# Kernel optimization log

Measured on AMD Instinct MI355X. Metric: run time of the kernel, lower is better.

The kernel has to match this reference:

```python
import jax, jax.numpy as jnp
import numpy as np

N, E, G = 8000, 128000, 4
C, NLM, NL = 64, 16, 4
NEL, NB, NH = 10, 8, 64
RMAX = 5.0
PCUT = 5.0
AVG_NEIGH = 16.0
SIGMA = 1.0
LBOX = 6.0
KR = 3
T = 2
LMAP = jnp.array([0, 1, 1, 1, 2, 2, 2, 2, 2, 3, 3, 3, 3, 3, 3, 3])


def _nvec():
    r = np.arange(-KR, KR + 1)
    n = np.stack(np.meshgrid(r, r, r, indexing='ij'), -1).reshape(-1, 3)
    n = n[np.any(n != 0, axis=1)]  # [342,3], k=0 excluded
    return jnp.asarray(n, jnp.float32)


def sph_harm(u):
    # component-normalized real spherical harmonics up to l=3, unit input u [E,3]
    x, y, z = u[:, 0], u[:, 1], u[:, 2]
    one = jnp.ones_like(x)
    c3, c5, c15 = 3.0 ** 0.5, 5.0 ** 0.5, 15.0 ** 0.5
    Y = [one,
         c3 * x, c3 * y, c3 * z,
         c15 * x * y, c15 * y * z, 0.5 * c5 * (3 * z * z - 1.0), c15 * x * z, 0.5 * c15 * (x * x - y * y),
         (35.0 / 8.0) ** 0.5 * y * (3 * x * x - y * y), 105.0 ** 0.5 * x * y * z,
         (21.0 / 8.0) ** 0.5 * y * (5 * z * z - 1.0), 0.5 * 7.0 ** 0.5 * z * (5 * z * z - 3.0),
         (21.0 / 8.0) ** 0.5 * x * (5 * z * z - 1.0), 0.5 * 105.0 ** 0.5 * z * (x * x - y * y),
         (35.0 / 8.0) ** 0.5 * x * (x * x - 3 * y * y)]
    return jnp.stack(Y, -1)  # [E,16]


def radial_basis(r):
    # Bessel basis * polynomial cutoff (MACE RadialEmbeddingBlock)
    u = r / RMAX
    n = jnp.arange(1, NB + 1, dtype=jnp.float32)
    bes = (2.0 / RMAX) ** 0.5 * jnp.sin(n[None, :] * jnp.pi * u[:, None]) / (r[:, None] + 1e-9)
    p = PCUT
    fc = 1.0 - 0.5 * (p + 1) * (p + 2) * u ** p + p * (p + 2) * u ** (p + 1) - 0.5 * p * (p + 1) * u ** (p + 2)
    fc = fc * (u < 1.0)
    return bes * fc[:, None]  # [E,8]


def setup_inputs() -> dict:
    key = jax.random.key(0)
    ks = jax.random.split(key, 24)

    def p(k, shape, fan_in):
        return jax.random.normal(k, shape, jnp.float32) / (fan_in ** 0.5)

    elem = jax.random.randint(ks[0], (N,), 0, NEL)
    inp = {
        'node_attrs': jax.nn.one_hot(elem, NEL, dtype=jnp.float32),
        'positions': jax.random.uniform(ks[1], (N, 3), jnp.float32) * LBOX,
        'shifts': jnp.zeros((E, 3), jnp.float32),
        'density_coefficients': jax.random.normal(ks[2], (N, 1), jnp.float32) * 0.1,
        'cell': jnp.tile(jnp.eye(3, dtype=jnp.float32) * LBOX, (G, 1, 1)),
        'rcell': jnp.tile(jnp.eye(3, dtype=jnp.float32) / LBOX, (G, 1, 1)),
        'volume': jnp.full((G,), LBOX ** 3, jnp.float32),
        'edge_index': jax.random.randint(ks[3], (2, E), 0, N),
        'batch': jnp.repeat(jnp.arange(G), N // G),
        'emb_W': p(ks[4], (NEL, C), NEL),
        'q_coef': p(ks[5], (T, C), 1),
        'rad_W1': p(ks[6], (T, NB, NH), NB),
        'rad_W2': p(ks[7], (T, NH, NH), NH),
        'rad_W3': p(ks[8], (T, NH, NH), NH),
        'rad_W4': p(ks[9], (T, NH, C * NL), NH),
        'lin_up': p(ks[10], (T, NL, C, C), C),
        'lin_out': p(ks[11], (T, NL, C, C), C),
        'W_sc': p(ks[12], (T, NEL, C, C), C),
        'Wp': p(ks[13], (T, 3, C, C), C),
        'W_read0': p(ks[14], (C,), C),
        'Wread1_a': p(ks[15], (C, 16), C),
        'Wread1_b': p(ks[16], (16,), 16),
        'Wq_read': p(ks[17], (T, C), C),
        'atomic_E': jax.random.normal(ks[18], (NEL,), jnp.float32),
    }
    return inp


def reference(node_attrs, positions, shifts, density_coefficients, cell, rcell, volume,
              edge_index, batch, emb_W, q_coef, rad_W1, rad_W2, rad_W3, rad_W4,
              lin_up, lin_out, W_sc, Wp, W_read0, Wread1_a, Wread1_b, Wq_read, atomic_E):
    sender, receiver = edge_index[0], edge_index[1]
    vec = positions[receiver] - positions[sender] + shifts
    r = jnp.linalg.norm(vec, axis=-1)
    Y = sph_harm(vec / (r[:, None] + 1e-9))      # [E,16]
    ef = radial_basis(r)                          # [E,8]

    q = density_coefficients                      # [N,1], max_l=0 multipoles
    feats = jnp.zeros((N, C, NLM), jnp.float32).at[:, :, 0].set(node_attrs @ emb_W)
    e0 = jax.ops.segment_sum(node_attrs @ atomic_E, batch, G)
    energies = [e0]

    for t in range(T):
        # charge-coefficient injection (charge_coefs_linears)
        feats = feats.at[:, :, 0].add(q * q_coef[t][None, :])
        # per-l linear up
        h = jnp.einsum('ncl,lcd->ndl', feats, lin_up[t][LMAP])
        # radial MLP -> per-edge, per-channel, per-l tensor-product weights
        w = jax.nn.silu(ef @ rad_W1[t])
        w = jax.nn.silu(w @ rad_W2[t])
        w = jax.nn.silu(w @ rad_W3[t])
        w = (w @ rad_W4[t]).reshape(E, C, NL)[:, :, LMAP]   # [E,C,16]
        # depthwise equivariant TP message: gather -> contract -> modulate
        hj = h[sender]                                       # [E,C,16]
        s_e = jnp.einsum('ecl,el->ec', hj, Y)                # edge invariant
        m = w * (Y[:, None, :] * s_e[:, :, None])            # [E,C,16]
        A = jax.ops.segment_sum(m, receiver, N) / AVG_NEIGH  # scatter-reduce
        A = jnp.einsum('ncl,lcd->ndl', A, lin_out[t][LMAP])
        # element-dependent residual (self-connection)
        wn = jnp.einsum('nk,kcd->ncd', node_attrs, W_sc[t])
        sc = jnp.einsum('ncd,ncl->ndl', wn, feats)
        # product block: correlation-3 symmetric-contraction surrogate
        s1 = jnp.sum(A * A, axis=2)                           # [N,C]
        out = (jnp.einsum('ncl,cd->ndl', A, Wp[t, 0])
               + jnp.einsum('ncl,cd->ndl', A * s1[:, :, None], Wp[t, 1])
               + jnp.einsum('ncl,cd->ndl', A * (s1 * s1)[:, :, None], Wp[t, 2]))
        feats = out + sc
        # readout
        if t == T - 1:
            node_e = jax.nn.silu(feats[:, :, 0] @ Wread1_a) @ Wread1_b
        else:
            node_e = feats[:, :, 0] @ W_read0
        node_e = node_e + q[:, 0] * (feats[:, :, 0] @ Wq_read[t])
        energies.append(jax.ops.segment_sum(node_e, batch, G))

    # k-space (Ewald-like) electrostatics with Gaussian-smeared charges
    nv = _nvec()                                              # [K,3]
    kvec = 2.0 * jnp.pi * jnp.einsum('kj,gji->gki', nv, rcell)  # [G,K,3]
    k2 = jnp.sum(kvec * kvec, -1)                             # [G,K]
    phase = jnp.einsum('ni,nki->nk', positions, kvec[batch])  # [N,K]
    Sr = jax.ops.segment_sum(q * jnp.cos(phase), batch, G)
    Si = jax.ops.segment_sum(q * jnp.sin(phase), batch, G)
    filt = jnp.exp(-0.5 * SIGMA * SIGMA * k2) / k2
    Ees = (2.0 * jnp.pi / volume) * jnp.sum(filt * (Sr * Sr + Si * Si), axis=1)

    total_energy = jnp.sum(jnp.stack(energies, -1), -1) + Ees
    total_charge = jax.ops.segment_sum(q[:, 0], batch, G)
    dipole = jax.ops.segment_sum(q * positions, batch, G)
    return total_energy, total_charge, dipole
```

## Files before the change

### kernel.cpp

```cpp
#include <hip/hip_runtime.h>
#include <hip/hip_bf16.h>

constexpr int N    = 8000;
constexpr int E    = 128000;
constexpr int G    = 4;
constexpr int NEL  = 10;
constexpr int NGR  = N / G;
constexpr int NC   = N * 64;
constexpr int NK   = 342;
constexpr float RMAX = 5.0f;
constexpr int HS = 72;
constexpr int WT_T = 25088;

typedef __bf16 bf16x8 __attribute__((ext_vector_type(8)));
typedef float  f32x4v __attribute__((ext_vector_type(4)));
typedef unsigned short u16x8 __attribute__((ext_vector_type(8)));

__device__ __forceinline__ int lmap_rt(int l) { return (l >= 1) + (l >= 4) + (l >= 9); }
__device__ __forceinline__ float silu(float x) { return x / (1.f + __expf(-x)); }
__device__ __forceinline__ float bf2f(unsigned short u) { return __uint_as_float(((unsigned)u) << 16); }
__device__ __forceinline__ unsigned short f2bf(float f) {
    __hip_bfloat16 h = __float2bfloat16(f);
    return *(unsigned short*)&h;
}

__device__ __forceinline__ void mfma_stage(const unsigned short* hsrc, const unsigned short* wt,
                                           int m0, int lane, f32x4v acc[4], bool k8only)
{
    const int quad = lane >> 4;
    const int idx  = lane & 15;
    bf16x8 bz;
    #pragma unroll
    for (int i = 0; i < 8; ++i) bz[i] = (__bf16)0.f;
    bf16x8 a0 = bz, a1 = bz;
    const int mrow = m0 + idx;
    if (k8only) {
        if (quad == 0) a0 = *(const bf16x8*)&hsrc[mrow * HS];
    } else {
        a0 = *(const bf16x8*)&hsrc[mrow * HS + (quad << 3)];
        a1 = *(const bf16x8*)&hsrc[mrow * HS + 32 + (quad << 3)];
    }
    #pragma unroll
    for (int c4 = 0; c4 < 4; ++c4) {
        const int nrow = (c4 << 4) + idx;
        if (k8only) {
            bf16x8 b0 = bz;
            if (quad == 0) b0 = *(const bf16x8*)&wt[nrow * HS];
            acc[c4] = __builtin_amdgcn_mfma_f32_16x16x32_bf16(a0, b0, acc[c4], 0, 0, 0);
        } else {
            const bf16x8 b0 = *(const bf16x8*)&wt[nrow * HS + (quad << 3)];
            const bf16x8 b1 = *(const bf16x8*)&wt[nrow * HS + 32 + (quad << 3)];
            acc[c4] = __builtin_amdgcn_mfma_f32_16x16x32_bf16(a0, b0, acc[c4], 0, 0, 0);
            acc[c4] = __builtin_amdgcn_mfma_f32_16x16x32_bf16(a1, b1, acc[c4], 0, 0, 0);
        }
    }
}

__global__ __launch_bounds__(256) void k_init(const float* __restrict__ na,
    const float* __restrict__ q, const float* __restrict__ pos,
    const int* __restrict__ batch, const float* __restrict__ aE,
    int* __restrict__ elem, int* __restrict__ counts, float* __restrict__ acc)
{
    __shared__ float s[G * 5];
    if (threadIdx.x < G * 5) s[threadIdx.x] = 0.f;
    __syncthreads();
    const int n = blockIdx.x * 256 + threadIdx.x;
    if (n < N) {
        int el = 0; float best = na[n * NEL];
        #pragma unroll
        for (int j = 1; j < NEL; ++j) { float v = na[n * NEL + j]; if (v > best) { best = v; el = j; } }
        elem[n] = el;
        atomicAdd(&counts[el], 1);
        const int g = batch[n];
        const float qn = q[n];
        atomicAdd(&s[g * 5 + 0], aE[el]);
        atomicAdd(&s[g * 5 + 1], qn);
        atomicAdd(&s[g * 5 + 2], qn * pos[n * 3 + 0]);
        atomicAdd(&s[g * 5 + 3], qn * pos[n * 3 + 1]);
        atomicAdd(&s[g * 5 + 4], qn * pos[n * 3 + 2]);
    }
    __syncthreads();
    if (threadIdx.x < G * 5) atomicAdd(&acc[threadIdx.x], s[threadIdx.x]);
}

__global__ __launch_bounds__(256) void k_feat0(const int* __restrict__ elem,
    const float* __restrict__ embW, float* __restrict__ F)
{
    const int i = blockIdx.x * 256 + threadIdx.x;
    if (i < NC) F[i] = embW[elem[i >> 6] * 64 + (i & 63)];
}

__global__ void k_offs(const int* __restrict__ counts, int* __restrict__ offs)
{
    if (threadIdx.x == 0 && blockIdx.x == 0) {
        int o = 0;
        for (int j = 0; j < NEL; ++j) { offs[j] = o; o += (counts[j] + 63) & ~63; }
        offs[NEL] = o;
    }
}
__global__ __launch_bounds__(256) void k_scatter(const int* __restrict__ elem,
    const int* __restrict__ offs, int* __restrict__ cursor, int* __restrict__ perm)
{
    const int n = blockIdx.x * 256 + threadIdx.x;
    if (n < N) {
        const int el = elem[n];
        const int p = atomicAdd(&cursor[el], 1);
        perm[offs[el] + p] = n;
    }
}

__global__ __launch_bounds__(256) void k_gcnt(const int* __restrict__ ei, int* __restrict__ cnt)
{
    const int e = blockIdx.x * 256 + threadIdx.x;
    if (e < E) atomicAdd(&cnt[ei[E + e]], 1);
}
__global__ __launch_bounds__(1024) void k_goff(const int* __restrict__ cnt, int* __restrict__ roff)
{
    __shared__ int part[1024];
    const int t = threadIdx.x;
    const int base = t * 8;
    int loc[8];
    int s = 0;
    #pragma unroll
    for (int i = 0; i < 8; ++i) { loc[i] = s; s += (base + i < N) ? cnt[base + i] : 0; }
    part[t] = s;
    __syncthreads();
    for (int d = 1; d < 1024; d <<= 1) {
        const int v = (t >= d) ? part[t - d] : 0;
        __syncthreads();
        part[t] += v;
        __syncthreads();
    }
    const int excl = (t == 0) ? 0 : part[t - 1];
    #pragma unroll
    for (int i = 0; i < 8; ++i) if (base + i < N) roff[base + i] = excl + loc[i];
    if (t == 0) roff[N] = E;
}
__global__ __launch_bounds__(256) void k_gscat(const int* __restrict__ ei,
    const int* __restrict__ roff, int* __restrict__ cur, int* __restrict__ elist)
{
    const int e = blockIdx.x * 256 + threadIdx.x;
    if (e < E) {
        const int rv = ei[E + e];
        const int p = atomicAdd(&cur[rv], 1);
        elist[roff[rv] + p] = e;
    }
}

__global__ __launch_bounds__(256) void k_geom(const float* __restrict__ pos,
    const float* __restrict__ shifts, const int* __restrict__ ei,
    const int* __restrict__ elist, float4* __restrict__ geomv, int* __restrict__ spck)
{
    const int j = blockIdx.x * 256 + threadIdx.x;
    if (j >= E) return;
    const int e = elist[j];
    const int s = ei[e], rv = ei[E + e];
    const float dx = pos[rv * 3 + 0] - pos[s * 3 + 0] + shifts[e * 3 + 0];
    const float dy = pos[rv * 3 + 1] - pos[s * 3 + 1] + shifts[e * 3 + 1];
    const float dz = pos[rv * 3 + 2] - pos[s * 3 + 2] + shifts[e * 3 + 2];
    const float r = sqrtf(dx * dx + dy * dy + dz * dz);
    const float inv = 1.f / (r + 1e-9f);
    float4 g;
    g.x = dx * inv; g.y = dy * inv; g.z = dz * inv; g.w = r;
    geomv[j] = g;
    spck[j] = s;
}

__global__ __launch_bounds__(256) void k_wprep_all(const float* __restrict__ rW1,
    const float* __restrict__ rW2, const float* __restrict__ rW3,
    const float* __restrict__ rW4, const float* __restrict__ Wp,
    const float* __restrict__ lup, const float* __restrict__ lout,
    const float* __restrict__ Wsc,
    unsigned short* __restrict__ WT, unsigned short* __restrict__ WpT,
    unsigned short* __restrict__ WlupT, unsigned short* __restrict__ WloutT,
    unsigned short* __restrict__ WscT)
{
    const int gidx = blockIdx.x * 256 + threadIdx.x;
    if (gidx < 2 * WT_T) {
        const int t = gidx / WT_T;
        const int r = gidx % WT_T;
        float v;
        if (r < 512) {
            const int n = r >> 3, k = r & 7;
            v = rW1[t * 512 + k * 64 + n];
        } else if (r < 4608) {
            const int i = r - 512, n = i >> 6, k = i & 63;
            v = rW2[t * 4096 + k * 64 + n];
        } else if (r < 8704) {
            const int i = r - 4608, n = i >> 6, k = i & 63;
            v = rW3[t * 4096 + k * 64 + n];
        } else {
            const int i = r - 8704, n = i >> 6, k = i & 63;
            v = rW4[t * 16384 + k * 256 + n];
        }
        WT[gidx] = f2bf(v);
    } else if (gidx < 2 * WT_T + 24576) {
        const int idx = gidx - 2 * WT_T;
        const int i  = idx & 4095;
        const int d = i >> 6, c = i & 63;
        WpT[idx] = f2bf(Wp[(size_t)(idx >> 12) * 4096 + c * 64 + d]);
    } else if (gidx < 2 * WT_T + 24576 + 32768) {
        const int idx = gidx - (2 * WT_T + 24576);
        const int i = idx & 4095, d = i >> 6, c = i & 63;
        WlupT[idx] = f2bf(lup[(idx >> 12) * 4096 + c * 64 + d]);
    } else if (gidx < 2 * WT_T + 24576 + 65536) {
        const int idx = gidx - (2 * WT_T + 24576 + 32768);
        const int i = idx & 4095, d = i >> 6, c = i & 63;
        WloutT[idx] = f2bf(lout[(idx >> 12) * 4096 + c * 64 + d]);
    } else if (gidx < 2 * WT_T + 24576 + 65536 + 81920) {
        const int idx = gidx - (2 * WT_T + 24576 + 65536);
        const int i = idx & 4095, d = i >> 6, c = i & 63;
        WscT[idx] = f2bf(Wsc[(idx >> 12) * 4096 + c * 64 + d]);
    }
}

__global__ __launch_bounds__(256) void k_lgemm_hb(float* __restrict__ F,
    const float* __restrict__ q, const float* __restrict__ qc,
    const unsigned short* __restrict__ WT, unsigned short* __restrict__ Hb)
{
    __shared__ unsigned short Xb[64 * HS];
    __shared__ unsigned short Wt[64 * HS];
    const int l  = blockIdx.y;
    const int nb = blockIdx.x << 6;
    const int t  = threadIdx.x;
    const int lane = t & 63;
    const int m0   = (t >> 6) << 4;
    const int quad = lane >> 4;
    const int idx  = lane & 15;
    const int prow = t >> 2, pkb = (t & 3) << 4;
    float* Xp = F + (size_t)l * NC + (size_t)nb * 64;
    if (l == 0) {
        #pragma unroll
        for (int k = 0; k < 16; ++k) {
            const int i = t + (k << 8);
            float v = Xp[i] + q[nb + (i >> 6)] * qc[i & 63];
            Xp[i] = v;
            Xb[(i >> 6) * HS + (i & 63)] = f2bf(v);
        }
    } else {
        #pragma unroll
        for (int k = 0; k < 16; ++k) {
            const int i = t + (k << 8);
            Xb[(i >> 6) * HS + (i & 63)] = f2bf(Xp[i]);
        }
    }
    const unsigned short* W = WT + lmap_rt(l) * 4096;
    *(u16x8*)&Wt[prow * HS + pkb]     = *(const u16x8*)&W[prow * 64 + pkb];
    *(u16x8*)&Wt[prow * HS + pkb + 8] = *(const u16x8*)&W[prow * 64 + pkb + 8];
    __syncthreads();
    f32x4v acc[4];
    #pragma unroll
    for (int c = 0; c < 4; ++c) { acc[c][0] = 0.f; acc[c][1] = 0.f; acc[c][2] = 0.f; acc[c][3] = 0.f; }
    mfma_stage(Xb, Wt, m0, lane, acc, false);
    #pragma unroll
    for (int c4 = 0; c4 < 4; ++c4) {
        #pragma unroll
        for (int r = 0; r < 4; ++r) {
            const int n = nb + m0 + (quad << 2) + r;
            const int col = (c4 << 4) + idx;
            Hb[(size_t)n * 1024 + (l << 6) + col] = f2bf(acc[c4][r]);
        }
    }
}

__global__ __launch_bounds__(256) void k_hbT(const unsigned short* __restrict__ Hb,
    unsigned short* __restrict__ HbT)
{
    const int n = (blockIdx.x << 2) + (threadIdx.x >> 6);
    const int c = threadIdx.x & 63;
    u16x8 a, b;
    #pragma unroll
    for (int l = 0; l < 8; ++l) {
        a[l] = Hb[(size_t)n * 1024 + (l << 6) + c];
        b[l] = Hb[(size_t)n * 1024 + ((l + 8) << 6) + c];
    }
    *(u16x8*)&HbT[(size_t)n * 1024 + c * 16]     = a;
    *(u16x8*)&HbT[(size_t)n * 1024 + c * 16 + 8] = b;
}

__global__ __launch_bounds__(256) void k_lgemm(const float* __restrict__ X,
    const unsigned short* __restrict__ WT, float* __restrict__ Out)
{
    __shared__ unsigned short Xb[64 * HS];
    __shared__ unsigned short Wt[64 * HS];
    const int l  = blockIdx.y;
    const int nb = blockIdx.x << 6;
    const int t  = threadIdx.x;
    const int lane = t & 63;
    const int m0   = (t >> 6) << 4;
    const int quad = lane >> 4;
    const int idx  = lane & 15;
    const int prow = t >> 2, pkb = (t & 3) << 4;
    const float* Xp = X + (size_t)l * NC + (size_t)nb * 64;
    #pragma unroll
    for (int k = 0; k < 16; ++k) {
        const int i = t + (k << 8);
        Xb[(i >> 6) * HS + (i & 63)] = f2bf(Xp[i]);
    }
    const unsigned short* W = WT + lmap_rt(l) * 4096;
    *(u16x8*)&Wt[prow * HS + pkb]     = *(const u16x8*)&W[prow * 64 + pkb];
    *(u16x8*)&Wt[prow * HS + pkb + 8] = *(const u16x8*)&W[prow * 64 + pkb + 8];
    __syncthreads();
    f32x4v acc[4];
    #pragma unroll
    for (int c = 0; c < 4; ++c) { acc[c][0] = 0.f; acc[c][1] = 0.f; acc[c][2] = 0.f; acc[c][3] = 0.f; }
    mfma_stage(Xb, Wt, m0, lane, acc, false);
    float* Op = Out + (size_t)l * NC + (size_t)nb * 64;
    #pragma unroll
    for (int c4 = 0; c4 < 4; ++c4) {
        #pragma unroll
        for (int r = 0; r < 4; ++r) {
            const int row = m0 + (quad << 2) + r;
            Op[(row << 6) + (c4 << 4) + idx] = acc[c4][r];
        }
    }
}

__global__ __launch_bounds__(256) void k_sc(const float* __restrict__ F,
    const unsigned short* __restrict__ WscT, const int* __restrict__ perm,
    const int* __restrict__ elem, float* __restrict__ Out)
{
    __shared__ unsigned short Xb[64 * HS];
    __shared__ unsigned short Wt[64 * HS];
    __shared__ int rows[64];
    const int l  = blockIdx.y;
    const int tb = blockIdx.x << 6;
    const int t  = threadIdx.x;
    if (t < 64) rows[t] = perm[tb + t];
    __syncthreads();
    if (rows[0] < 0) return;
    const int lane = t & 63;
    const int m0   = (t >> 6) << 4;
    const int quad = lane >> 4;
    const int idx  = lane & 15;
    const int prow = t >> 2, pkb = (t & 3) << 4;
    const unsigned short* W = WscT + elem[rows[0]] * 4096;
    *(u16x8*)&Wt[prow * HS + pkb]     = *(const u16x8*)&W[prow * 64 + pkb];
    *(u16x8*)&Wt[prow * HS + pkb + 8] = *(const u16x8*)&W[prow * 64 + pkb + 8];
    #pragma unroll
    for (int k = 0; k < 16; ++k) {
        const int i = t + (k << 8);
        const int rr = i >> 6, cc = i & 63;
        const int n = rows[rr];
        Xb[rr * HS + cc] = (n >= 0) ? f2bf(F[(size_t)l * NC + (size_t)n * 64 + cc]) : (unsigned short)0;
    }
    __syncthreads();
    f32x4v acc[4];
    #pragma unroll
    for (int c = 0; c < 4; ++c) { acc[c][0] = 0.f; acc[c][1] = 0.f; acc[c][2] = 0.f; acc[c][3] = 0.f; }
    mfma_stage(Xb, Wt, m0, lane, acc, false);
    #pragma unroll
    for (int c4 = 0; c4 < 4; ++c4) {
        #pragma unroll
        for (int r = 0; r < 4; ++r) {
            const int n = rows[m0 + (quad << 2) + r];
            if (n >= 0) Out[(size_t)l * NC + (size_t)n * 64 + (c4 << 4) + idx] = acc[c4][r];
        }
    }
}

__global__ __launch_bounds__(256) void k_wgemm(const float4* __restrict__ geomv,
    const unsigned short* __restrict__ WT, unsigned short* __restrict__ wout)
{
    __shared__ unsigned short hbf[64 * HS];
    __shared__ unsigned short wtb[2][64 * HS];
    __shared__ unsigned short outS[64 * HS];
    const int t = threadIdx.x;
    const int lane = t & 63;
    const int wid  = t >> 6;
    const int m0   = wid << 4;
    const int quad = lane >> 4;
    const int idx  = lane & 15;
    const int j0 = blockIdx.x << 6;
    if (t < 64) {
        const float r = geomv[j0 + t].w;
        const float u  = r * 0.2f;
        const float u2 = u * u, u5 = u2 * u2 * u;
        const float fc = 1.f - 21.f * u5 + 35.f * u5 * u - 15.f * u5 * u2;
        float pref = 0.63245553f * fc / (r + 1e-9f);
        if (u >= 1.f) pref = 0.f;
        const float piu = 3.14159265358979f * u;
        #pragma unroll
        for (int b = 0; b < 8; ++b) hbf[t * HS + b] = f2bf(__sinf((float)(b + 1) * piu) * pref);
    }
    {
        const int n = t >> 2, k = (t & 3) << 1;
        wtb[0][n * HS + k]     = WT[n * 8 + k];
        wtb[0][n * HS + k + 1] = WT[n * 8 + k + 1];
    }
    const int prow = t >> 2, pkb = (t & 3) << 4;
    u16x8 pf0, pf1;
    pf0 = *(const u16x8*)&WT[512 + prow * 64 + pkb];
    pf1 = *(const u16x8*)&WT[512 + prow * 64 + pkb + 8];
    __syncthreads();
    f32x4v acc[4];
    #pragma unroll
    for (int c = 0; c < 4; ++c) { acc[c][0] = 0.f; acc[c][1] = 0.f; acc[c][2] = 0.f; acc[c][3] = 0.f; }
    mfma_stage(hbf, wtb[0], m0, lane, acc, true);
    __syncthreads();
    #pragma unroll
    for (int c4 = 0; c4 < 4; ++c4)
        #pragma unroll
        for (int r = 0; r < 4; ++r)
            hbf[(m0 + (quad << 2) + r) * HS + (c4 << 4) + idx] = f2bf(silu(acc[c4][r]));
    *(u16x8*)&wtb[1][prow * HS + pkb]     = pf0;
    *(u16x8*)&wtb[1][prow * HS + pkb + 8] = pf1;
    pf0 = *(const u16x8*)&WT[4608 + prow * 64 + pkb];
    pf1 = *(const u16x8*)&WT[4608 + prow * 64 + pkb + 8];
    __syncthreads();
    #pragma unroll
    for (int c = 0; c < 4; ++c) { acc[c][0] = 0.f; acc[c][1] = 0.f; acc[c][2] = 0.f; acc[c][3] = 0.f; }
    mfma_stage(hbf, wtb[1], m0, lane, acc, false);
    __syncthreads();
    #pragma unroll
    for (int c4 = 0; c4 < 4; ++c4)
        #pragma unroll
        for (int r = 0; r < 4; ++r)
            hbf[(m0 + (quad << 2) + r) * HS + (c4 << 4) + idx] = f2bf(silu(acc[c4][r]));
    *(u16x8*)&wtb[0][prow * HS + pkb]     = pf0;
    *(u16x8*)&wtb[0][prow * HS + pkb + 8] = pf1;
    pf0 = *(const u16x8*)&WT[8704 + prow * 64 + pkb];
    pf1 = *(const u16x8*)&WT[8704 + prow * 64 + pkb + 8];
    __syncthreads();
    #pragma unroll
    for (int c = 0; c < 4; ++c) { acc[c][0] = 0.f; acc[c][1] = 0.f; acc[c][2] = 0.f; acc[c][3] = 0.f; }
    mfma_stage(hbf, wtb[0], m0, lane, acc, false);
    __syncthreads();
    #pragma unroll
    for (int c4 = 0; c4 < 4; ++c4)
        #pragma unroll
        for (int r = 0; r < 4; ++r)
            hbf[(m0 + (quad << 2) + r) * HS + (c4 << 4) + idx] = f2bf(silu(acc[c4][r]));
    *(u16x8*)&wtb[1][prow * HS + pkb]     = pf0;
    *(u16x8*)&wtb[1][prow * HS + pkb + 8] = pf1;
    pf0 = *(const u16x8*)&WT[8704 + 4096 + prow * 64 + pkb];
    pf1 = *(const u16x8*)&WT[8704 + 4096 + prow * 64 + pkb + 8];
    __syncthreads();
    int cur = 1;
    for (int c = 0; c < 4; ++c) {
        #pragma unroll
        for (int cc = 0; cc < 4; ++cc) { acc[cc][0] = 0.f; acc[cc][1] = 0.f; acc[cc][2] = 0.f; acc[cc][3] = 0.f; }
        mfma_stage(hbf, wtb[cur], m0, lane, acc, false);
        __syncthreads();
        #pragma unroll
        for (int c4 = 0; c4 < 4; ++c4)
            #pragma unroll
            for (int r = 0; r < 4; ++r)
                outS[(m0 + (quad << 2) + r) * HS + (c4 << 4) + idx] = f2bf(acc[c4][r]);
        if (c < 3) {
            *(u16x8*)&wtb[1 - cur][prow * HS + pkb]     = pf0;
            *(u16x8*)&wtb[1 - cur][prow * HS + pkb + 8] = pf1;
            if (c < 2) {
                pf0 = *(const u16x8*)&WT[8704 + (c + 2) * 4096 + prow * 64 + pkb];
                pf1 = *(const u16x8*)&WT[8704 + (c + 2) * 4096 + prow * 64 + pkb + 8];
            }
        }
        __syncthreads();
        *(u16x8*)&wout[(size_t)(j0 + prow) * 256 + (c << 6) + pkb]     = *(const u16x8*)&outS[prow * HS + pkb];
        *(u16x8*)&wout[(size_t)(j0 + prow) * 256 + (c << 6) + pkb + 8] = *(const u16x8*)&outS[prow * HS + pkb + 8];
        cur ^= 1;
    }
}

__global__ __launch_bounds__(256) void k_agg(const float4* __restrict__ geomv,
    const int* __restrict__ spck,
    const unsigned short* __restrict__ HbT, const unsigned short* __restrict__ wb,
    const int* __restrict__ roff, float* __restrict__ A)
{
    const int lane = threadIdx.x & 63;
    const int n = (blockIdx.x << 2) + (threadIdx.x >> 6);
    const int ja = roff[n], jb2 = roff[n + 1];
    float accv[16];
    #pragma unroll
    for (int l = 0; l < 16; ++l) accv[l] = 0.f;
    constexpr int LM[16] = {0,1,1,1,2,2,2,2,2,3,3,3,3,3,3,3};
    if (ja < jb2) {
        const int jlast = jb2 - 1;
        int j1c = ja + 1 < jlast ? ja + 1 : jlast;
        int j2c = ja + 2 < jlast ? ja + 2 : jlast;
        float4 g0 = geomv[ja],  g1 = geomv[j1c],  g2 = geomv[j2c];
        ushort4 w0 = *(const ushort4*)&wb[(size_t)ja * 256 + (lane << 2)];
        ushort4 w1 = *(const ushort4*)&wb[(size_t)j1c * 256 + (lane << 2)];
        ushort4 w2 = *(const ushort4*)&wb[(size_t)j2c * 256 + (lane << 2)];
        int sB = spck[j1c], sC = spck[j2c];
        u16x8 hA, hB;
        {
            const int s0 = spck[ja];
            hA = *(const u16x8*)&HbT[(size_t)s0 * 1024 + lane * 16];
            hB = *(const u16x8*)&HbT[(size_t)s0 * 1024 + lane * 16 + 8];
        }
        for (int j = ja; j < jb2; ++j) {
            const float4 gc = g0;
            const ushort4 wc = w0;
            float hc[16];
            #pragma unroll
            for (int l = 0; l < 8; ++l) { hc[l] = bf2f(hA[l]); hc[l + 8] = bf2f(hB[l]); }
            g0 = g1; g1 = g2; w0 = w1; w1 = w2;
            const int sA = sB; sB = sC;
            hA = *(const u16x8*)&HbT[(size_t)sA * 1024 + lane * 16];
            hB = *(const u16x8*)&HbT[(size_t)sA * 1024 + lane * 16 + 8];
            const int j3 = j + 3 < jlast ? j + 3 : jlast;
            g2 = geomv[j3];
            w2 = *(const ushort4*)&wb[(size_t)j3 * 256 + (lane << 2)];
            sC = spck[j3];
            if (gc.w < RMAX) {
                const float x = gc.x, y = gc.y, z = gc.z;
                const float xx = x * x, yy = y * y, zz = z * z;
                float Y[16];
                Y[0] = 1.f;
                Y[1] = 1.7320508f * x;  Y[2] = 1.7320508f * y;  Y[3] = 1.7320508f * z;
                Y[4] = 3.8729833f * x * y;  Y[5] = 3.8729833f * y * z;
                Y[6] = 0.5f * 2.2360680f * (3.f * zz - 1.f);
                Y[7] = 3.8729833f * x * z;  Y[8] = 0.5f * 3.8729833f * (xx - yy);
                Y[9]  = 2.0916500f * y * (3.f * xx - yy);
                Y[10] = 10.2469508f * x * y * z;
                Y[11] = 1.6201852f * y * (5.f * zz - 1.f);
                Y[12] = 0.5f * 2.6457513f * z * (5.f * zz - 3.f);
                Y[13] = 1.6201852f * x * (5.f * zz - 1.f);
                Y[14] = 0.5f * 10.2469508f * z * (xx - yy);
                Y[15] = 2.0916500f * x * (xx - 3.f * yy);
                float se = 0.f;
                #pragma unroll
                for (int l = 0; l < 16; ++l) se += hc[l] * Y[l];
                se *= 0.0625f;
                const float wl[4] = { bf2f(wc.x) * se, bf2f(wc.y) * se, bf2f(wc.z) * se, bf2f(wc.w) * se };
                #pragma unroll
                for (int l = 0; l < 16; ++l) accv[l] += wl[LM[l]] * Y[l];
            }
        }
    }
    float* Ap = A + (size_t)n * 64 + lane;
    #pragma unroll
    for (int l = 0; l < 16; ++l) Ap[(size_t)l * NC] = accv[l];
}

__global__ __launch_bounds__(256) void k_s1(const float* __restrict__ H, float* __restrict__ s1)
{
    const int i = blockIdx.x * 256 + threadIdx.x;
    if (i < NC) {
        float s = 0.f;
        #pragma unroll
        for (int l = 0; l < 16; ++l) { const float a = H[(size_t)l * NC + i]; s += a * a; }
        s1[i] = s;
    }
}

__global__ __launch_bounds__(256) void k_out(const float* __restrict__ Ap,
    const float* __restrict__ s1, const unsigned short* __restrict__ WpT,
    const float* __restrict__ sc, float* __restrict__ F)
{
    __shared__ unsigned short Xb[64 * HS];
    __shared__ unsigned short Wt[64 * HS];
    const int l  = blockIdx.y;
    const int nb = blockIdx.x << 6;
    const int t  = threadIdx.x;
    const int lane = t & 63;
    const int m0   = (t >> 6) << 4;
    const int quad = lane >> 4;
    const int idx  = lane & 15;
    const int prow = t >> 2, pkb = (t & 3) << 4;
    const float* Xp = Ap + (size_t)l * NC + (size_t)nb * 64;
    float av[16], sv[16];
    #pragma unroll
    for (int k = 0; k < 16; ++k) {
        const int i = t + (k << 8);
        av[k] = Xp[i];
        sv[k] = s1[nb * 64 + i];
    }
    f32x4v acc[4];
    #pragma unroll
    for (int c = 0; c < 4; ++c) { acc[c][0] = 0.f; acc[c][1] = 0.f; acc[c][2] = 0.f; acc[c][3] = 0.f; }
    for (int p = 0; p < 3; ++p) {
        #pragma unroll
        for (int k = 0; k < 16; ++k) {
            const int i = t + (k << 8);
            Xb[(i >> 6) * HS + (i & 63)] = f2bf(av[k]);
            av[k] *= sv[k];
        }
        *(u16x8*)&Wt[prow * HS + pkb]     = *(const u16x8*)&WpT[p * 4096 + prow * 64 + pkb];
        *(u16x8*)&Wt[prow * HS + pkb + 8] = *(const u16x8*)&WpT[p * 4096 + prow * 64 + pkb + 8];
        __syncthreads();
        mfma_stage(Xb, Wt, m0, lane, acc, false);
        __syncthreads();
    }
    #pragma unroll
    for (int c4 = 0; c4 < 4; ++c4) {
        #pragma unroll
        for (int r = 0; r < 4; ++r) {
            const int row = m0 + (quad << 2) + r;
            const int col = (c4 << 4) + idx;
            const size_t id = (size_t)l * NC + (size_t)(nb + row) * 64 + col;
            F[id] = acc[c4][r] + sc[id];
        }
    }
}

__global__ __launch_bounds__(256) void k_read(const float* __restrict__ F,
    const float* __restrict__ q, const int* __restrict__ batch,
    const float* __restrict__ Wr0, const float* __restrict__ Wa,
    const float* __restrict__ Wb, const float* __restrict__ Wq,
    float* __restrict__ acc, int last)
{
    __shared__ float sred[G];
    if (threadIdx.x < G) sred[threadIdx.x] = 0.f;
    __syncthreads();
    const int n = blockIdx.x * 256 + threadIdx.x;
    if (n < N) {
        float a16[16];
        #pragma unroll
        for (int j = 0; j < 16; ++j) a16[j] = 0.f;
        float ar = 0.f, aq = 0.f;
        const float* f = F + (size_t)n * 64;
        for (int c = 0; c < 64; ++c) {
            const float fv = f[c];
            aq += fv * Wq[c];
            if (last) {
                #pragma unroll
                for (int j = 0; j < 16; ++j) a16[j] += fv * Wa[c * 16 + j];
            } else ar += fv * Wr0[c];
        }
        float en;
        if (last) {
            en = 0.f;
            #pragma unroll
            for (int j = 0; j < 16; ++j) en += silu(a16[j]) * Wb[j];
        } else en = ar;
        en += q[n] * aq;
        atomicAdd(&sred[batch[n]], en);
    }
    __syncthreads();
    if (threadIdx.x < G) atomicAdd(&acc[threadIdx.x * 5], sred[threadIdx.x]);
}

__global__ __launch_bounds__(256) void k_kvec(const float* __restrict__ rcell,
    float* __restrict__ kvec, float* __restrict__ k2)
{
    const int idx = blockIdx.x * 256 + threadIdx.x;
    if (idx >= G * NK) return;
    const int g = idx / NK, k = idx % NK;
    const int kk = k + (k >= 171 ? 1 : 0);
    const int a = kk / 49 - 3, b = (kk / 7) % 7 - 3, c = kk % 7 - 3;
    const float* rc = rcell + g * 9;
    float s = 0.f;
    #pragma unroll
    for (int i = 0; i < 3; ++i) {
        const float kv = 6.283185307f * ((float)a * rc[0 + i] + (float)b * rc[3 + i] + (float)c * rc[6 + i]);
        kvec[idx * 3 + i] = kv;
        s += kv * kv;
    }
    k2[idx] = s;
}

__global__ __launch_bounds__(256) void k_phase(const float* __restrict__ pos,
    const float* __restrict__ q, const float* __restrict__ kvec,
    float* __restrict__ Sr, float* __restrict__ Si)
{
    __shared__ float kvs[38 * 3];
    __shared__ float srs[38], sis[38];
    const int g = blockIdx.z, kc = blockIdx.x, ncb = blockIdx.y;
    const int kbase = kc * 38;
    if (threadIdx.x < 38 * 3) kvs[threadIdx.x] = kvec[((size_t)g * NK + kbase) * 3 + threadIdx.x];
    if (threadIdx.x < 38) { srs[threadIdx.x] = 0.f; sis[threadIdx.x] = 0.f; }
    __syncthreads();
    const int t = threadIdx.x;
    float px = 0.f, py = 0.f, pz = 0.f, qn = 0.f;
    if (t < 250) {
        const int n = g * NGR + ncb * 250 + t;
        px = pos[n * 3]; py = pos[n * 3 + 1]; pz = pos[n * 3 + 2]; qn = q[n];
    }
    const int lane = t & 63;
    for (int j = 0; j < 38; ++j) {
        const float ph = px * kvs[j * 3] + py * kvs[j * 3 + 1] + pz * kvs[j * 3 + 2];
        float sv, cv;
        __sincosf(ph, &sv, &cv);
        float vr = qn * cv, vi = qn * sv;
        #pragma unroll
        for (int o = 32; o > 0; o >>= 1) { vr += __shfl_down(vr, o, 64); vi += __shfl_down(vi, o, 64); }
        if (lane == 0) { atomicAdd(&srs[j], vr); atomicAdd(&sis[j], vi); }
    }
    __syncthreads();
    if (t < 38) {
        atomicAdd(&Sr[g * NK + kbase + t], srs[t]);
        atomicAdd(&Si[g * NK + kbase + t], sis[t]);
    }
}

__global__ __launch_bounds__(512) void k_final(const float* __restrict__ k2,
    const float* __restrict__ Sr, const float* __restrict__ Si,
    const float* __restrict__ vol, const float* __restrict__ acc,
    float* __restrict__ out)
{
    __shared__ float red[512];
    const int g = blockIdx.x, t = threadIdx.x;
    float v = 0.f;
    if (t < NK) {
        const float kk = k2[g * NK + t];
        const float sr = Sr[g * NK + t], si = Si[g * NK + t];
        v = __expf(-0.5f * kk) * (sr * sr + si * si) / kk;
    }
    red[t] = v;
    __syncthreads();
    for (int s2 = 256; s2 > 0; s2 >>= 1) {
        if (t < s2) red[t] += red[t + s2];
        __syncthreads();
    }
    if (t == 0) {
        const float Ees = 6.283185307f / vol[g] * red[0];
        out[g]     = acc[g * 5 + 0] + Ees;
        out[4 + g] = acc[g * 5 + 1];
        out[8 + g * 3 + 0] = acc[g * 5 + 2];
        out[8 + g * 3 + 1] = acc[g * 5 + 3];
        out[8 + g * 3 + 2] = acc[g * 5 + 4];
    }
}

extern "C" void kernel_launch(void* const* d_in, const int* in_sizes, int n_in,
                              void* d_out, int out_size, void* d_ws, size_t ws_size,
                              hipStream_t stream)
{
    const float* na    = (const float*)d_in[0];
    const float* pos   = (const float*)d_in[1];
    const float* shif  = (const float*)d_in[2];
    const float* q     = (const float*)d_in[3];
    const float* rcell = (const float*)d_in[5];
    const float* vol   = (const float*)d_in[6];
    const int*   ei    = (const int*)d_in[7];
    const int*   batch = (const int*)d_in[8];
    const float* embW  = (const float*)d_in[9];
    const float* qcoef = (const float*)d_in[10];
    const float* rW1   = (const float*)d_in[11];
    const float* rW2   = (const float*)d_in[12];
    const float* rW3   = (const float*)d_in[13];
    const float* rW4   = (const float*)d_in[14];
    const float* lup   = (const float*)d_in[15];
    const float* lout  = (const float*)d_in[16];
    const float* Wsc   = (const float*)d_in[17];
    const float* Wp    = (const float*)d_in[18];
    const float* Wr0   = (const float*)d_in[19];
    const float* Wa    = (const float*)d_in[20];
    const float* Wb    = (const float*)d_in[21];
    const float* Wq    = (const float*)d_in[22];
    const float* aE    = (const float*)d_in[23];
    float* out = (float*)d_out;

    float* wsf  = (float*)d_ws;
    float* F    = wsf;
    float* A    = F + 8192000;
    float* R    = A + 8192000;
    float* H2   = R;
    unsigned short* Hbtmp = (unsigned short*)A;
    unsigned short* HbT   = (unsigned short*)R;
    unsigned short* wb = (unsigned short*)(R + 4096000);
    float* s1   = R + 20480000;
    float* kvec = s1 + 512000;
    float* k2   = kvec + 4104;
    float* Sr   = k2 + 1368;
    float* Si   = Sr + 1368;
    float* acc  = Si + 1368;
    int*   elem = (int*)(acc + 32);
    int*   perm = elem + 8000;
    int*   counts = perm + 8640;
    int*   cursor = counts + 16;
    int*   offs   = cursor + 16;
    int*   roff   = offs + 16;
    int*   cnt    = roff + 8001;
    int*   cur    = cnt + 8000;
    int*   elist  = cur + 8000;
    unsigned short* WTb = (unsigned short*)(((uintptr_t)(elist + E) + 31) & ~(uintptr_t)31);
    unsigned short* WpT = WTb + 2 * WT_T;
    float4* geomv = (float4*)(WpT + 24576);
    int*    spck  = (int*)(geomv + E);
    unsigned short* WlupT  = (unsigned short*)(spck + E);
    unsigned short* WloutT = WlupT + 32768;
    unsigned short* WscT   = WloutT + 32768;

    hipMemsetAsync(F, 0, 8192000 * sizeof(float), stream);
    hipMemsetAsync(Sr, 0, (1368 * 2 + 32) * sizeof(float), stream);
    hipMemsetAsync(perm, 0xFF, 8640 * sizeof(int), stream);
    hipMemsetAsync(counts, 0, 32 * sizeof(int), stream);
    hipMemsetAsync(cnt, 0, 16000 * sizeof(int), stream);

    k_init<<<32, 256, 0, stream>>>(na, q, pos, batch, aE, elem, counts, acc);
    k_feat0<<<2000, 256, 0, stream>>>(elem, embW, F);
    k_offs<<<1, 64, 0, stream>>>(counts, offs);
    k_scatter<<<32, 256, 0, stream>>>(elem, offs, cursor, perm);
    k_gcnt<<<500, 256, 0, stream>>>(ei, cnt);
    k_goff<<<1, 1024, 0, stream>>>(cnt, roff);
    k_gscat<<<500, 256, 0, stream>>>(ei, roff, cur, elist);
    k_geom<<<500, 256, 0, stream>>>(pos, shif, ei, elist, geomv, spck);
    k_wprep_all<<<868, 256, 0, stream>>>(rW1, rW2, rW3, rW4, Wp, lup, lout, Wsc,
                                         WTb, WpT, WlupT, WloutT, WscT);
    k_kvec<<<6, 256, 0, stream>>>(rcell, kvec, k2);
    k_phase<<<dim3(9, 8, G), 256, 0, stream>>>(pos, q, kvec, Sr, Si);

    for (int t = 0; t < 2; ++t) {
        k_lgemm_hb<<<dim3(125, 16), 256, 0, stream>>>(F, q, qcoef + t * 64, WlupT + t * 16384, Hbtmp);
        k_hbT<<<2000, 256, 0, stream>>>(Hbtmp, HbT);
        k_wgemm<<<2000, 256, 0, stream>>>(geomv, WTb + t * WT_T, wb);
        k_agg<<<2000, 256, 0, stream>>>(geomv, spck, HbT, wb, roff, A);
        k_lgemm<<<dim3(125, 16), 256, 0, stream>>>(A, WloutT + t * 16384, H2);
        k_s1<<<2000, 256, 0, stream>>>(H2, s1);
        k_sc<<<dim3(135, 16), 256, 0, stream>>>(F, WscT + t * 40960, perm, elem, A);
        k_out<<<dim3(125, 16), 256, 0, stream>>>(H2, s1, WpT + t * 12288, A, F);
        k_read<<<32, 256, 0, stream>>>(F, q, batch, Wr0, Wa, Wb, Wq + t * 64, acc, t == 1);
    }
    k_final<<<G, 512, 0, stream>>>(k2, Sr, Si, vol, acc, out);
}
```

Baseline: 573.1 us.

## Fuse radial weight MLP with edge aggregation, keeping per-edge weights in LDS

```diff
diff --git a/kernel.cpp b/kernel.cpp
--- a/kernel.cpp
+++ b/kernel.cpp
@@ -10,6 +10,7 @@
 constexpr int NK   = 342;
 constexpr float RMAX = 5.0f;
 constexpr int HS = 72;
+constexpr int WS2 = 260;
 constexpr int WT_T = 25088;
 
 typedef __bf16 bf16x8 __attribute__((ext_vector_type(8)));
@@ -359,21 +360,41 @@
     }
 }
 
-__global__ __launch_bounds__(256) void k_wgemm(const float4* __restrict__ geomv,
-    const unsigned short* __restrict__ WT, unsigned short* __restrict__ wout)
+__global__ __launch_bounds__(256) void k_edge(const float4* __restrict__ geomv,
+    const int* __restrict__ spck, const unsigned short* __restrict__ WT,
+    const unsigned short* __restrict__ HbT, const int* __restrict__ roff,
+    float* __restrict__ A)
 {
     __shared__ unsigned short hbf[64 * HS];
-    __shared__ unsigned short wtb[2][64 * HS];
-    __shared__ unsigned short outS[64 * HS];
+    __shared__ unsigned short wtb[64 * HS];
+    __shared__ unsigned short wfull[64 * WS2];
+    __shared__ float geos[64 * 4];
+    __shared__ int   sps[64];
+    __shared__ int   rinfo[2];
     const int t = threadIdx.x;
     const int lane = t & 63;
     const int wid  = t >> 6;
     const int m0   = wid << 4;
     const int quad = lane >> 4;
     const int idx  = lane & 15;
-    const int j0 = blockIdx.x << 6;
+    const int prow = t >> 2, pkb = (t & 3) << 4;
+    const int w0 = blockIdx.x << 6;
+    const int w1 = w0 + 64;
+    if (t == 0) {
+        int lo = 0, hi = N - 1;
+        while (lo < hi) { const int mid = (lo + hi + 1) >> 1; if (roff[mid] <= w0) lo = mid; else hi = mid - 1; }
+        rinfo[0] = lo;
+    } else if (t == 1) {
+        const int w1m = w0 + 63;
+        int lo = 0, hi = N - 1;
+        while (lo < hi) { const int mid = (lo + hi + 1) >> 1; if (roff[mid] <= w1m) lo = mid; else hi = mid - 1; }
+        rinfo[1] = lo;
+    }
     if (t < 64) {
-        const float r = geomv[j0 + t].w;
+        const float4 g = geomv[w0 + t];
+        *(float4*)&geos[t * 4] = g;
+        sps[t] = spck[w0 + t];
+        const float r = g.w;
         const float u  = r * 0.2f;
         const float u2 = u * u, u5 = u2 * u2 * u;
         const float fc = 1.f - 21.f * u5 + 35.f * u5 * u - 15.f * u5 * u2;
@@ -385,126 +406,111 @@
     }
     {
         const int n = t >> 2, k = (t & 3) << 1;
-        wtb[0][n * HS + k]     = WT[n * 8 + k];
-        wtb[0][n * HS + k + 1] = WT[n * 8 + k + 1];
-    }
-    const int prow = t >> 2, pkb = (t & 3) << 4;
-    u16x8 pf0, pf1;
-    pf0 = *(const u16x8*)&WT[512 + prow * 64 + pkb];
-    pf1 = *(const u16x8*)&WT[512 + prow * 64 + pkb + 8];
+        wtb[n * HS + k]     = WT[n * 8 + k];
+        wtb[n * HS + k + 1] = WT[n * 8 + k + 1];
+    }
+    u16x8 pf0 = *(const u16x8*)&WT[512 + prow * 64 + pkb];
+    u16x8 pf1 = *(const u16x8*)&WT[512 + prow * 64 + pkb + 8];
     __syncthreads();
     f32x4v acc[4];
     #pragma unroll
     for (int c = 0; c < 4; ++c) { acc[c][0] = 0.f; acc[c][1] = 0.f; acc[c][2] = 0.f; acc[c][3] = 0.f; }
-    mfma_stage(hbf, wtb[0], m0, lane, acc, true);
+    mfma_stage(hbf, wtb, m0, lane, acc, true);
     __syncthreads();
     #pragma unroll
     for (int c4 = 0; c4 < 4; ++c4)
         #pragma unroll
         for (int r = 0; r < 4; ++r)
             hbf[(m0 + (quad << 2) + r) * HS + (c4 << 4) + idx] = f2bf(silu(acc[c4][r]));
-    *(u16x8*)&wtb[1][prow * HS + pkb]     = pf0;
-    *(u16x8*)&wtb[1][prow * HS + pkb + 8] = pf1;
+    *(u16x8*)&wtb[prow * HS + pkb]     = pf0;
+    *(u16x8*)&wtb[prow * HS + pkb + 8] = pf1;
     pf0 = *(const u16x8*)&WT[4608 + prow * 64 + pkb];
     pf1 = *(const u16x8*)&WT[4608 + prow * 64 + pkb + 8];
     __syncthreads();
     #pragma unroll
     for (int c = 0; c < 4; ++c) { acc[c][0] = 0.f; acc[c][1] = 0.f; acc[c][2] = 0.f; acc[c][3] = 0.f; }
-    mfma_stage(hbf, wtb[1], m0, lane, acc, false);
+    mfma_stage(hbf, wtb, m0, lane, acc, false);
     __syncthreads();
     #pragma unroll
     for (int c4 = 0; c4 < 4; ++c4)
         #pragma unroll
         for (int r = 0; r < 4; ++r)
             hbf[(m0 + (quad << 2) + r) * HS + (c4 << 4) + idx] = f2bf(silu(acc[c4][r]));
-    *(u16x8*)&wtb[0][prow * HS + pkb]     = pf0;
-    *(u16x8*)&wtb[0][prow * HS + pkb + 8] = pf1;
+    *(u16x8*)&wtb[prow * HS + pkb]     = pf0;
+    *(u16x8*)&wtb[prow * HS + pkb + 8] = pf1;
     pf0 = *(const u16x8*)&WT[8704 + prow * 64 + pkb];
     pf1 = *(const u16x8*)&WT[8704 + prow * 64 + pkb + 8];
     __syncthreads();
     #pragma unroll
     for (int c = 0; c < 4; ++c) { acc[c][0] = 0.f; acc[c][1] = 0.f; acc[c][2] = 0.f; acc[c][3] = 0.f; }
-    mfma_stage(hbf, wtb[0], m0, lane, acc, false);
+    mfma_stage(hbf, wtb, m0, lane, acc, false);
     __syncthreads();
     #pragma unroll
     for (int c4 = 0; c4 < 4; ++c4)
         #pragma unroll
         for (int r = 0; r < 4; ++r)
             hbf[(m0 + (quad << 2) + r) * HS + (c4 << 4) + idx] = f2bf(silu(acc[c4][r]));
-    *(u16x8*)&wtb[1][prow * HS + pkb]     = pf0;
-    *(u16x8*)&wtb[1][prow * HS + pkb + 8] = pf1;
+    *(u16x8*)&wtb[prow * HS + pkb]     = pf0;
+    *(u16x8*)&wtb[prow * HS + pkb + 8] = pf1;
     pf0 = *(const u16x8*)&WT[8704 + 4096 + prow * 64 + pkb];
     pf1 = *(const u16x8*)&WT[8704 + 4096 + prow * 64 + pkb + 8];
     __syncthreads();
-    int cur = 1;
-    for (int c = 0; c < 4; ++c) {
-        #pragma unroll
-        for (int cc = 0; cc < 4; ++cc) { acc[cc][0] = 0.f; acc[cc][1] = 0.f; acc[cc][2] = 0.f; acc[cc][3] = 0.f; }
-        mfma_stage(hbf, wtb[cur], m0, lane, acc, false);
+    for (int cc = 0; cc < 4; ++cc) {
+        #pragma unroll
+        for (int c = 0; c < 4; ++c) { acc[c][0] = 0.f; acc[c][1] = 0.f; acc[c][2] = 0.f; acc[c][3] = 0.f; }
+        mfma_stage(hbf, wtb, m0, lane, acc, false);
         __syncthreads();
         #pragma unroll
         for (int c4 = 0; c4 < 4; ++c4)
             #pragma unroll
             for (int r = 0; r < 4; ++r)
-                outS[(m0 + (quad << 2) + r) * HS + (c4 << 4) + idx] = f2bf(acc[c4][r]);
-        if (c < 3) {
-            *(u16x8*)&wtb[1 - cur][prow * HS + pkb]     = pf0;
-            *(u16x8*)&wtb[1 - cur][prow * HS + pkb + 8] = pf1;
-            if (c < 2) {
-                pf0 = *(const u16x8*)&WT[8704 + (c + 2) * 4096 + prow * 64 + pkb];
-                pf1 = *(const u16x8*)&WT[8704 + (c + 2) * 4096 + prow * 64 + pkb + 8];
+                wfull[(m0 + (quad << 2) + r) * WS2 + (cc << 6) + (c4 << 4) + idx] = f2bf(acc[c4][r]);
+        if (cc < 3) {
+            *(u16x8*)&wtb[prow * HS + pkb]     = pf0;
+            *(u16x8*)&wtb[prow * HS + pkb + 8] = pf1;
+            if (cc < 2) {
+                pf0 = *(const u16x8*)&WT[8704 + (cc + 2) * 4096 + prow * 64 + pkb];
+                pf1 = *(const u16x8*)&WT[8704 + (cc + 2) * 4096 + prow * 64 + pkb + 8];
             }
         }
         __syncthreads();
-        *(u16x8*)&wout[(size_t)(j0 + prow) * 256 + (c << 6) + pkb]     = *(const u16x8*)&outS[prow * HS + pkb];
-        *(u16x8*)&wout[(size_t)(j0 + prow) * 256 + (c << 6) + pkb + 8] = *(const u16x8*)&outS[prow * HS + pkb + 8];
-        cur ^= 1;
-    }
-}
-
-__global__ __launch_bounds__(256) void k_agg(const float4* __restrict__ geomv,
-    const int* __restrict__ spck,
-    const unsigned short* __restrict__ HbT, const unsigned short* __restrict__ wb,
-    const int* __restrict__ roff, float* __restrict__ A)
-{
-    const int lane = threadIdx.x & 63;
-    const int n = (blockIdx.x << 2) + (threadIdx.x >> 6);
-    const int ja = roff[n], jb2 = roff[n + 1];
-    float accv[16];
-    #pragma unroll
-    for (int l = 0; l < 16; ++l) accv[l] = 0.f;
+    }
+    const int r0 = rinfo[0], r1 = rinfo[1];
     constexpr int LM[16] = {0,1,1,1,2,2,2,2,2,3,3,3,3,3,3,3};
-    if (ja < jb2) {
-        const int jlast = jb2 - 1;
-        int j1c = ja + 1 < jlast ? ja + 1 : jlast;
-        int j2c = ja + 2 < jlast ? ja + 2 : jlast;
-        float4 g0 = geomv[ja],  g1 = geomv[j1c],  g2 = geomv[j2c];
-        ushort4 w0 = *(const ushort4*)&wb[(size_t)ja * 256 + (lane << 2)];
-        ushort4 w1 = *(const ushort4*)&wb[(size_t)j1c * 256 + (lane << 2)];
-        ushort4 w2 = *(const ushort4*)&wb[(size_t)j2c * 256 + (lane << 2)];
-        int sB = spck[j1c], sC = spck[j2c];
-        u16x8 hA, hB;
-        {
-            const int s0 = spck[ja];
-            hA = *(const u16x8*)&HbT[(size_t)s0 * 1024 + lane * 16];
-            hB = *(const u16x8*)&HbT[(size_t)s0 * 1024 + lane * 16 + 8];
-        }
-        for (int j = ja; j < jb2; ++j) {
-            const float4 gc = g0;
-            const ushort4 wc = w0;
-            float hc[16];
-            #pragma unroll
-            for (int l = 0; l < 8; ++l) { hc[l] = bf2f(hA[l]); hc[l + 8] = bf2f(hB[l]); }
-            g0 = g1; g1 = g2; w0 = w1; w1 = w2;
-            const int sA = sB; sB = sC;
-            hA = *(const u16x8*)&HbT[(size_t)sA * 1024 + lane * 16];
-            hB = *(const u16x8*)&HbT[(size_t)sA * 1024 + lane * 16 + 8];
-            const int j3 = j + 3 < jlast ? j + 3 : jlast;
-            g2 = geomv[j3];
-            w2 = *(const ushort4*)&wb[(size_t)j3 * 256 + (lane << 2)];
-            sC = spck[j3];
-            if (gc.w < RMAX) {
-                const float x = gc.x, y = gc.y, z = gc.z;
+    for (int r = r0 + wid; r <= r1; r += 4) {
+        const int ra = roff[r], rb = roff[r + 1];
+        const int ja = ra > w0 ? ra : w0;
+        const int jb = rb < w1 ? rb : w1;
+        float a16[16];
+        #pragma unroll
+        for (int l = 0; l < 16; ++l) a16[l] = 0.f;
+        if (ja < jb) {
+            u16x8 hA0, hB0, hA1, hB1;
+            {
+                const int s = sps[ja - w0];
+                hA0 = *(const u16x8*)&HbT[(size_t)s * 1024 + lane * 16];
+                hB0 = *(const u16x8*)&HbT[(size_t)s * 1024 + lane * 16 + 8];
+            }
+            hA1 = hA0; hB1 = hB0;
+            if (ja + 1 < jb) {
+                const int s = sps[ja + 1 - w0];
+                hA1 = *(const u16x8*)&HbT[(size_t)s * 1024 + lane * 16];
+                hB1 = *(const u16x8*)&HbT[(size_t)s * 1024 + lane * 16 + 8];
+            }
+            for (int j = ja; j < jb; ++j) {
+                const int jj = j - w0;
+                float hc[16];
+                #pragma unroll
+                for (int l = 0; l < 8; ++l) { hc[l] = bf2f(hA0[l]); hc[l + 8] = bf2f(hB0[l]); }
+                hA0 = hA1; hB0 = hB1;
+                if (j + 2 < jb) {
+                    const int s = sps[jj + 2];
+                    hA1 = *(const u16x8*)&HbT[(size_t)s * 1024 + lane * 16];
+                    hB1 = *(const u16x8*)&HbT[(size_t)s * 1024 + lane * 16 + 8];
+                }
+                const float gr = geos[jj * 4 + 3];
+                if (gr >= RMAX) continue;
+                const float x = geos[jj * 4], y = geos[jj * 4 + 1], z = geos[jj * 4 + 2];
                 const float xx = x * x, yy = y * y, zz = z * z;
                 float Y[16];
                 Y[0] = 1.f;
@@ -523,15 +529,21 @@
                 #pragma unroll
                 for (int l = 0; l < 16; ++l) se += hc[l] * Y[l];
                 se *= 0.0625f;
-                const float wl[4] = { bf2f(wc.x) * se, bf2f(wc.y) * se, bf2f(wc.z) * se, bf2f(wc.w) * se };
+                const ushort4 wq = *(const ushort4*)&wfull[jj * WS2 + (lane << 2)];
+                const float wl[4] = { bf2f(wq.x) * se, bf2f(wq.y) * se, bf2f(wq.z) * se, bf2f(wq.w) * se };
                 #pragma unroll
-                for (int l = 0; l < 16; ++l) accv[l] += wl[LM[l]] * Y[l];
+                for (int l = 0; l < 16; ++l) a16[l] += wl[LM[l]] * Y[l];
             }
         }
-    }
-    float* Ap = A + (size_t)n * 64 + lane;
-    #pragma unroll
-    for (int l = 0; l < 16; ++l) Ap[(size_t)l * NC] = accv[l];
+        float* Ap = A + (size_t)r * 64 + lane;
+        if (ra >= w0 && rb <= w1) {
+            #pragma unroll
+            for (int l = 0; l < 16; ++l) Ap[(size_t)l * NC] = a16[l];
+        } else {
+            #pragma unroll
+            for (int l = 0; l < 16; ++l) atomicAdd(&Ap[(size_t)l * NC], a16[l]);
+        }
+    }
 }
 
 __global__ __launch_bounds__(256) void k_s1(const float* __restrict__ H, float* __restrict__ s1)
@@ -748,9 +760,8 @@
     float* A    = F + 8192000;
     float* R    = A + 8192000;
     float* H2   = R;
-    unsigned short* Hbtmp = (unsigned short*)A;
     unsigned short* HbT   = (unsigned short*)R;
-    unsigned short* wb = (unsigned short*)(R + 4096000);
+    unsigned short* Hbtmp = (unsigned short*)(R + 4096000);
     float* s1   = R + 20480000;
     float* kvec = s1 + 512000;
     float* k2   = kvec + 4104;
@@ -796,8 +807,8 @@
     for (int t = 0; t < 2; ++t) {
         k_lgemm_hb<<<dim3(125, 16), 256, 0, stream>>>(F, q, qcoef + t * 64, WlupT + t * 16384, Hbtmp);
         k_hbT<<<2000, 256, 0, stream>>>(Hbtmp, HbT);
-        k_wgemm<<<2000, 256, 0, stream>>>(geomv, WTb + t * WT_T, wb);
-        k_agg<<<2000, 256, 0, stream>>>(geomv, spck, HbT, wb, roff, A);
+        hipMemsetAsync(A, 0, 8192000 * sizeof(float), stream);
+        k_edge<<<2000, 256, 0, stream>>>(geomv, spck, WTb + t * WT_T, HbT, roff, A);
         k_lgemm<<<dim3(125, 16), 256, 0, stream>>>(A, WloutT + t * 16384, H2);
         k_s1<<<2000, 256, 0, stream>>>(H2, s1);
         k_sc<<<dim3(135, 16), 256, 0, stream>>>(F, WscT + t * 40960, perm, elem, A);
```

After: 564.3 us. Within noise of the previous version (-1.5%).
